# Optimization experiments

Hardware: AMD Instinct MI355X
Metric: run time of the kernel (lower is better)

The kernel has to match this reference:

```python
import jax, jax.numpy as jnp
import numpy as np

N = 50000   # nodes
E = 800000  # edges
D = 128     # input feature dim
HID = 64    # hidden dim
NEG_SLOPE = 0.2


def setup_inputs() -> dict:
    key = jax.random.key(0)
    ks = jax.random.split(key, 12)
    s = 0.1
    x = jax.random.normal(ks[0], (N, D), jnp.float32)
    edge_index = jax.random.randint(ks[1], (2, E), 0, N, dtype=jnp.int64)
    # layer 1: GATConv(128 -> 64, heads=2, concat=False)
    W1 = jax.random.normal(ks[2], (D, 2 * HID), jnp.float32) * s
    a_src1 = jax.random.normal(ks[3], (2, HID), jnp.float32) * s
    a_dst1 = jax.random.normal(ks[4], (2, HID), jnp.float32) * s
    b1 = jnp.zeros((HID,), jnp.float32)
    # layer 2: GATConv(64 -> 64, heads=1, concat=False)
    W2 = jax.random.normal(ks[5], (HID, HID), jnp.float32) * s
    a_src2 = jax.random.normal(ks[6], (1, HID), jnp.float32) * s
    a_dst2 = jax.random.normal(ks[7], (1, HID), jnp.float32) * s
    b2 = jnp.zeros((HID,), jnp.float32)
    # classifier Linear(64 -> 2)
    Wc = jax.random.normal(ks[8], (HID, 2), jnp.float32) * s
    bc = jnp.zeros((2,), jnp.float32)
    return {"x": x, "edge_index": edge_index, "W1": W1, "a_src1": a_src1,
            "a_dst1": a_dst1, "b1": b1, "W2": W2, "a_src2": a_src2,
            "a_dst2": a_dst2, "b2": b2, "Wc": Wc, "bc": bc}


def _gat_layer(x, src, dst, W, a_s, a_d, b, n):
    """PyG GATConv (concat=False -> mean over heads), eval mode."""
    H, C = a_s.shape
    h = (x @ W).reshape(n, H, C)                      # [N,H,C]
    alpha_s = jnp.sum(h * a_s, axis=-1)               # [N,H]
    alpha_d = jnp.sum(h * a_d, axis=-1)               # [N,H]
    e = jax.nn.leaky_relu(alpha_s[src] + alpha_d[dst], NEG_SLOPE)  # [E,H]
    # segment softmax over incoming edges of each target node
    m = jax.ops.segment_max(e, dst, num_segments=n)   # [N,H]
    e = jnp.exp(e - m[dst])
    denom = jax.ops.segment_sum(e, dst, num_segments=n)
    alpha = e / (denom[dst] + 1e-16)                  # [E,H]
    msg = h[src] * alpha[:, :, None]                  # [E,H,C]
    out = jax.ops.segment_sum(msg, dst, num_segments=n)  # [N,H,C]
    return out.mean(axis=1) + b                       # [N,C]


def reference(x, edge_index, W1, a_src1, a_dst1, b1, W2, a_src2, a_dst2, b2, Wc, bc):
    n = x.shape[0]
    loops = jnp.arange(n, dtype=edge_index.dtype)     # PyG add_self_loops=True
    src = jnp.concatenate([edge_index[0], loops])
    dst = jnp.concatenate([edge_index[1], loops])
    h = jax.nn.elu(_gat_layer(x, src, dst, W1, a_src1, a_dst1, b1, n))
    h = jax.nn.elu(_gat_layer(h, src, dst, W2, a_src2, a_dst2, b2, n))
    logits = h @ Wc + bc
    return jax.nn.log_softmax(logits, axis=1)
```

## Files before the change

kernel.cpp:

```cpp
#include <hip/hip_runtime.h>
#include <math.h>

#define NN 50000
#define NE 800000
#define NT (NE + NN)
#define NBUCK 196
#define BE 4096
#define NBLK_B ((NT + BE - 1) / BE)
#define CAP 6144
#define NBLK_G ((NN + 63) / 64)

typedef short bf16x8 __attribute__((ext_vector_type(8)));
typedef float f32x4 __attribute__((ext_vector_type(4)));
union U16x8 { uint4 u; bf16x8 s; };

__device__ __forceinline__ unsigned pk_bf16x2(float x, float y) {
  unsigned ux = __float_as_uint(x); ux = ux + 0x7FFFu + ((ux >> 16) & 1u);
  unsigned uy = __float_as_uint(y); uy = uy + 0x7FFFu + ((uy >> 16) & 1u);
  return (ux >> 16) | (uy & 0xFFFF0000u);
}
__device__ __forceinline__ unsigned short bf16_1(float x) {
  unsigned u = __float_as_uint(x); u = u + 0x7FFFu + ((u >> 16) & 1u);
  return (unsigned short)(u >> 16);
}
__device__ __forceinline__ float blo(unsigned v) { return __uint_as_float(v << 16); }
__device__ __forceinline__ float bhi(unsigned v) { return __uint_as_float(v & 0xFFFF0000u); }

__global__ __launch_bounds__(256) void k_prep(const float* __restrict__ W1, const float* __restrict__ W2,
                                              unsigned short* __restrict__ w1f,
                                              unsigned short* __restrict__ w2f,
                                              int* __restrict__ bcur) {
  int i = blockIdx.x * 256 + threadIdx.x;
  if (i < NBUCK) bcur[i] = i * CAP;
  if (i < 128 * 128) {
    int k = i >> 7, col = i & 127;
    int ct = col >> 4, kt = k >> 5, lane = (((k >> 3) & 3) << 4) | (col & 15), j = k & 7;
    w1f[(((ct << 2) | kt) * 64 + lane) * 8 + j] = bf16_1(W1[i]);
  } else if (i < 128 * 128 + 64 * 64) {
    int e = i - 128 * 128;
    int k = e >> 6, col = e & 63;
    int ct = col >> 4, kt = k >> 5, lane = (((k >> 3) & 3) << 4) | (col & 15), j = k & 7;
    w2f[(((ct << 1) | kt) * 64 + lane) * 8 + j] = bf16_1(W2[e]);
  }
}

__global__ __launch_bounds__(256) void k_gb(
    const int* __restrict__ src, const int* __restrict__ dst,
    int* __restrict__ bcur, unsigned* __restrict__ staging,
    const float* __restrict__ x, const unsigned short* __restrict__ w1f,
    const float* __restrict__ asw_g, const float* __restrict__ adw_g,
    unsigned short* __restrict__ h1b, float* __restrict__ as1, float* __restrict__ ad1) {
  __shared__ int hist[NBUCK];
  __shared__ int base[NBUCK];
  if (blockIdx.x < NBLK_B) {
    const int t = threadIdx.x;
    const int e0 = blockIdx.x * BE;
    if (t < NBUCK) hist[t] = 0;
    __syncthreads();
    for (int j = t; j < BE; j += 256) {
      int i = e0 + j;
      if (i >= NT) break;
      int d = (i < NE) ? dst[i] : (i - NE);
      atomicAdd(&hist[d >> 8], 1);
    }
    __syncthreads();
    if (t < NBUCK) {
      int c = hist[t];
      base[t] = c ? atomicAdd(&bcur[t], c) : 0;
      hist[t] = 0;
    }
    __syncthreads();
    for (int j = t; j < BE; j += 256) {
      int i = e0 + j;
      if (i >= NT) break;
      int s, d;
      if (i < NE) { s = src[i]; d = dst[i]; } else { s = d = i - NE; }
      int b = d >> 8;
      int off = atomicAdd(&hist[b], 1);
      staging[base[b] + off] = ((unsigned)d << 16) | (unsigned)s;
    }
    return;
  }
  const int bid = blockIdx.x - NBLK_B;
  const int t = threadIdx.x;
  const int wid = t >> 6, l = t & 63;
  const int lr = l & 15, lg = l >> 4;
  const int arow = bid * 64 + wid * 16 + lr;
  const bool aok = arow < NN;

  float asw_t[8], adw_t[8];
#pragma unroll
  for (int ct = 0; ct < 8; ++ct) {
    asw_t[ct] = asw_g[ct * 16 + lr];
    adw_t[ct] = adw_g[ct * 16 + lr];
  }

  f32x4 acc[8];
#pragma unroll
  for (int ct = 0; ct < 8; ++ct) acc[ct] = (f32x4){0.f, 0.f, 0.f, 0.f};

#pragma unroll
  for (int kt = 0; kt < 4; ++kt) {
    U16x8 a;
    if (aok) {
      const float* xp = &x[(long long)arow * 128 + kt * 32 + lg * 8];
      float4 f0 = *(const float4*)xp;
      float4 f1 = *(const float4*)(xp + 4);
      a.u.x = pk_bf16x2(f0.x, f0.y); a.u.y = pk_bf16x2(f0.z, f0.w);
      a.u.z = pk_bf16x2(f1.x, f1.y); a.u.w = pk_bf16x2(f1.z, f1.w);
    } else {
      a.u = make_uint4(0, 0, 0, 0);
    }
#pragma unroll
    for (int ct = 0; ct < 8; ++ct) {
      U16x8 b;
      b.u = *(const uint4*)&w1f[(((ct << 2) | kt) * 64 + l) * 8];
      acc[ct] = __builtin_amdgcn_mfma_f32_16x16x32_bf16(a.s, b.s, acc[ct], 0, 0, 0);
    }
  }

  const int gr0 = bid * 64 + wid * 16 + lg * 4;
#pragma unroll
  for (int reg = 0; reg < 4; ++reg) {
    int grow = gr0 + reg;
    bool ok = grow < NN;
    float s0 = 0.f, s1 = 0.f, d0 = 0.f, d1 = 0.f;
#pragma unroll
    for (int ct = 0; ct < 8; ++ct) {
      float v = acc[ct][reg];
      if (ok) h1b[(long long)grow * 128 + ct * 16 + lr] = bf16_1(v);
      if (ct < 4) { s0 += v * asw_t[ct]; d0 += v * adw_t[ct]; }
      else        { s1 += v * asw_t[ct]; d1 += v * adw_t[ct]; }
    }
#pragma unroll
    for (int off = 1; off < 16; off <<= 1) {
      s0 += __shfl_xor(s0, off); d0 += __shfl_xor(d0, off);
      s1 += __shfl_xor(s1, off); d1 += __shfl_xor(d1, off);
    }
    if (ok && lr == 0) {
      as1[grow * 2] = s0; as1[grow * 2 + 1] = s1;
      ad1[grow * 2] = d0; ad1[grow * 2 + 1] = d1;
    }
  }
}

__global__ __launch_bounds__(256) void k_scatter2(const unsigned* __restrict__ staging,
                                                  const int* __restrict__ bcur,
                                                  int* __restrict__ rowptr,
                                                  unsigned short* __restrict__ csr16) {
  __shared__ int lcnt[256];
  __shared__ int wsum[4];
  __shared__ int sOff, sTot;
  const int b = blockIdx.x;
  const int t = threadIdx.x;
  const int nlo = b << 8;
  const int l = t & 63, w = t >> 6;

  int bc = (t < NBUCK) ? bcur[t] - t * CAP : 0;
  int sc = bc;
#pragma unroll
  for (int off = 1; off < 64; off <<= 1) {
    int u = __shfl_up(sc, off);
    if (l >= off) sc += u;
  }
  if (l == 63) wsum[w] = sc;
  __syncthreads();
  {
    int wo = 0;
    for (int i = 0; i < w; ++i) wo += wsum[i];
    int incl = sc + wo;
    if (t == b) sOff = incl - bc;
    if (t == 255) sTot = incl;
  }
  lcnt[t] = 0;
  __syncthreads();

  const int s0 = b * CAP;
  const int cnt = bcur[b] - s0;
  for (int k = t; k < cnt; k += 256)
    atomicAdd(&lcnt[(int)(staging[s0 + k] >> 16) - nlo], 1);
  __syncthreads();
  int v = lcnt[t];
  int sc2 = v;
#pragma unroll
  for (int off = 1; off < 64; off <<= 1) {
    int u = __shfl_up(sc2, off);
    if (l >= off) sc2 += u;
  }
  __syncthreads();
  if (l == 63) wsum[w] = sc2;
  __syncthreads();
  int wo = 0;
  for (int i = 0; i < w; ++i) wo += wsum[i];
  const int base = sOff + sc2 + wo - v;
  if (nlo + t < NN) rowptr[nlo + t] = base;
  if (b == NBUCK - 1 && t == 0) rowptr[NN] = sTot;
  __syncthreads();
  lcnt[t] = base;
  __syncthreads();
  for (int k = t; k < cnt; k += 256) {
    unsigned e = staging[s0 + k];
    int d = (int)(e >> 16) - nlo;
    int pos = atomicAdd(&lcnt[d], 1);
    csr16[pos] = (unsigned short)(e & 0xFFFFu);
  }
}

__global__ __launch_bounds__(256) void k_gat1(
    const int* __restrict__ rowptr, const unsigned short* __restrict__ csr16,
    const unsigned* __restrict__ h1u, const float2* __restrict__ as1,
    const float2* __restrict__ ad1, const float* __restrict__ b1,
    unsigned* __restrict__ out1b) {
  __shared__ float2 sw[4][2][64];
  const int t = threadIdx.x;
  const int wv = t >> 6;
  const int n = blockIdx.x * 4 + wv;
  if (n >= NN) return;
  const int p = t & 63;
  const int h = p >> 5;
  const int beg = rowptr[n], end = rowptr[n + 1];
  const int deg = end - beg;
  const float2 adn = ad1[n];

  float acc0 = 0.f, acc1 = 0.f;
  float inv;

  if (deg <= 64) {
    int s = 0; float e0 = -1e30f, e1 = -1e30f;
    if (p < deg) {
      s = csr16[beg + p];
      float2 a = as1[s];
      e0 = a.x + adn.x; e0 = fmaxf(e0, 0.2f * e0);
      e1 = a.y + adn.y; e1 = fmaxf(e1, 0.2f * e1);
    }
    float m0 = e0, m1 = e1;
#pragma unroll
    for (int off = 1; off < 64; off <<= 1) {
      m0 = fmaxf(m0, __shfl_xor(m0, off));
      m1 = fmaxf(m1, __shfl_xor(m1, off));
    }
    float w0 = (p < deg) ? __expf(e0 - m0) : 0.f;
    float w1 = (p < deg) ? __expf(e1 - m1) : 0.f;
    float d0 = w0, d1 = w1;
#pragma unroll
    for (int off = 1; off < 64; off <<= 1) {
      d0 += __shfl_xor(d0, off);
      d1 += __shfl_xor(d1, off);
    }
    sw[wv][0][p] = make_float2(__int_as_float(s), w0);
    sw[wv][1][p] = make_float2(__int_as_float(s), w1);
    __builtin_amdgcn_wave_barrier();
    inv = 1.f / ((h ? d1 : d0) + 1e-16f);

    int j = 0;
    for (; j + 8 <= deg; j += 8) {
      float2 a[8]; unsigned v[8];
#pragma unroll
      for (int u = 0; u < 8; ++u) a[u] = sw[wv][h][j + u];
#pragma unroll
      for (int u = 0; u < 8; ++u) v[u] = h1u[(__float_as_int(a[u].x) << 6) + p];
#pragma unroll
      for (int u = 0; u < 8; ++u) {
        acc0 += a[u].y * blo(v[u]);
        acc1 += a[u].y * bhi(v[u]);
      }
    }
    if (j + 4 <= deg) {
      float2 a[4]; unsigned v[4];
#pragma unroll
      for (int u = 0; u < 4; ++u) a[u] = sw[wv][h][j + u];
#pragma unroll
      for (int u = 0; u < 4; ++u) v[u] = h1u[(__float_as_int(a[u].x) << 6) + p];
#pragma unroll
      for (int u = 0; u < 4; ++u) {
        acc0 += a[u].y * blo(v[u]);
        acc1 += a[u].y * bhi(v[u]);
      }
      j += 4;
    }
    for (; j < deg; ++j) {
      float2 a = sw[wv][h][j];
      unsigned v = h1u[(__float_as_int(a.x) << 6) + p];
      acc0 += a.y * blo(v); acc1 += a.y * bhi(v);
    }
  } else {
    float m0 = -1e30f, d0 = 0.f, m1 = -1e30f, d1 = 0.f;
    for (int k = beg + p; k < end; k += 64) {
      float2 a = as1[csr16[k]];
      float e0 = a.x + adn.x; e0 = fmaxf(e0, 0.2f * e0);
      float e1 = a.y + adn.y; e1 = fmaxf(e1, 0.2f * e1);
      if (e0 > m0) { d0 *= __expf(m0 - e0); m0 = e0; }
      d0 += __expf(e0 - m0);
      if (e1 > m1) { d1 *= __expf(m1 - e1); m1 = e1; }
      d1 += __expf(e1 - m1);
    }
#pragma unroll
    for (int off = 1; off < 64; off <<= 1) {
      float mo = __shfl_xor(m0, off), dd = __shfl_xor(d0, off);
      float mn = fmaxf(m0, mo);
      d0 = d0 * __expf(m0 - mn) + dd * __expf(mo - mn);
      m0 = mn;
      mo = __shfl_xor(m1, off); dd = __shfl_xor(d1, off);
      mn = fmaxf(m1, mo);
      d1 = d1 * __expf(m1 - mn) + dd * __expf(mo - mn);
      m1 = mn;
    }
    inv = 1.f / ((h ? d1 : d0) + 1e-16f);
    for (int c0 = beg; c0 < end; c0 += 64) {
      int nc = end - c0; if (nc > 64) nc = 64;
      int s = 0; float w0 = 0.f, w1 = 0.f;
      if (p < nc) {
        s = csr16[c0 + p];
        float2 a = as1[s];
        float e0 = a.x + adn.x; e0 = fmaxf(e0, 0.2f * e0);
        float e1 = a.y + adn.y; e1 = fmaxf(e1, 0.2f * e1);
        w0 = __expf(e0 - m0);
        w1 = __expf(e1 - m1);
      }
      __builtin_amdgcn_wave_barrier();
      sw[wv][0][p] = make_float2(__int_as_float(s), w0);
      sw[wv][1][p] = make_float2(__int_as_float(s), w1);
      __builtin_amdgcn_wave_barrier();
      for (int j = 0; j < nc; ++j) {
        float2 a = sw[wv][h][j];
        unsigned v = h1u[(__float_as_int(a.x) << 6) + p];
        acc0 += a.y * blo(v); acc1 += a.y * bhi(v);
      }
      __builtin_amdgcn_wave_barrier();
    }
  }

  acc0 *= inv; acc1 *= inv;
  acc0 += __shfl_xor(acc0, 32);
  acc1 += __shfl_xor(acc1, 32);
  if (p < 32) {
    float u0 = 0.5f * acc0 + b1[2 * p];
    float u1 = 0.5f * acc1 + b1[2 * p + 1];
    u0 = u0 > 0.f ? u0 : expm1f(u0);
    u1 = u1 > 0.f ? u1 : expm1f(u1);
    out1b[n * 32 + p] = pk_bf16x2(u0, u1);
  }
}

__global__ __launch_bounds__(256) void k_gemm2(
    const unsigned short* __restrict__ in_b, const unsigned short* __restrict__ w2f,
    const float* __restrict__ asw_g, const float* __restrict__ adw_g,
    unsigned short* __restrict__ h2b, float* __restrict__ as2, float* __restrict__ ad2) {
  const int t = threadIdx.x;
  const int wid = t >> 6, l = t & 63;
  const int lr = l & 15, lg = l >> 4;
  const int arow = blockIdx.x * 64 + wid * 16 + lr;
  const bool aok = arow < NN;

  float asw_t[4], adw_t[4];
#pragma unroll
  for (int ct = 0; ct < 4; ++ct) {
    asw_t[ct] = asw_g[ct * 16 + lr];
    adw_t[ct] = adw_g[ct * 16 + lr];
  }

  f32x4 acc[4];
#pragma unroll
  for (int ct = 0; ct < 4; ++ct) acc[ct] = (f32x4){0.f, 0.f, 0.f, 0.f};

#pragma unroll
  for (int kt = 0; kt < 2; ++kt) {
    U16x8 a;
    if (aok) a.u = *(const uint4*)&in_b[(long long)arow * 64 + kt * 32 + lg * 8];
    else a.u = make_uint4(0, 0, 0, 0);
#pragma unroll
    for (int ct = 0; ct < 4; ++ct) {
      U16x8 b;
      b.u = *(const uint4*)&w2f[(((ct << 1) | kt) * 64 + l) * 8];
      acc[ct] = __builtin_amdgcn_mfma_f32_16x16x32_bf16(a.s, b.s, acc[ct], 0, 0, 0);
    }
  }

  const int gr0 = blockIdx.x * 64 + wid * 16 + lg * 4;
#pragma unroll
  for (int reg = 0; reg < 4; ++reg) {
    int grow = gr0 + reg;
    bool ok = grow < NN;
    float s0 = 0.f, d0 = 0.f;
#pragma unroll
    for (int ct = 0; ct < 4; ++ct) {
      float v = acc[ct][reg];
      if (ok) h2b[(long long)grow * 64 + ct * 16 + lr] = bf16_1(v);
      s0 += v * asw_t[ct]; d0 += v * adw_t[ct];
    }
#pragma unroll
    for (int off = 1; off < 16; off <<= 1) {
      s0 += __shfl_xor(s0, off); d0 += __shfl_xor(d0, off);
    }
    if (ok && lr == 0) { as2[grow] = s0; ad2[grow] = d0; }
  }
}

__global__ __launch_bounds__(256) void k_gat2(
    const int* __restrict__ rowptr, const unsigned short* __restrict__ csr16,
    const unsigned* __restrict__ h2u, const float* __restrict__ as2,
    const float* __restrict__ ad2, const float* __restrict__ b2,
    const float* __restrict__ Wc, const float* __restrict__ bc,
    float* __restrict__ out) {
  __shared__ float2 sw[4][64];
  const int t = threadIdx.x;
  const int wv = t >> 6;
  const int n = blockIdx.x * 4 + wv;
  if (n >= NN) return;
  const int p = t & 63;
  const int half = p >> 5;
  const int q = p & 31;
  const int beg = rowptr[n], end = rowptr[n + 1];
  const int deg = end - beg;
  const float adn = ad2[n];

  float acc0 = 0.f, acc1 = 0.f;
  float inv;

  if (deg <= 64) {
    int s = 0; float e = -1e30f;
    if (p < deg) {
      s = csr16[beg + p];
      e = as2[s] + adn;
      e = fmaxf(e, 0.2f * e);
    }
    float m = e;
#pragma unroll
    for (int off = 1; off < 64; off <<= 1) m = fmaxf(m, __shfl_xor(m, off));
    float w = (p < deg) ? __expf(e - m) : 0.f;
    float d = w;
#pragma unroll
    for (int off = 1; off < 64; off <<= 1) d += __shfl_xor(d, off);
    sw[wv][p] = make_float2(__int_as_float(s), w);
    __builtin_amdgcn_wave_barrier();
    inv = 1.f / (d + 1e-16f);

    int niter = (deg + 1) >> 1;
    int i = 0;
    for (; i + 4 <= niter; i += 4) {
      float2 a[4]; unsigned v[4];
#pragma unroll
      for (int u = 0; u < 4; ++u) a[u] = sw[wv][2 * (i + u) + half];
#pragma unroll
      for (int u = 0; u < 4; ++u) v[u] = h2u[(__float_as_int(a[u].x) << 5) + q];
#pragma unroll
      for (int u = 0; u < 4; ++u) {
        acc0 += a[u].y * blo(v[u]);
        acc1 += a[u].y * bhi(v[u]);
      }
    }
    if (i + 2 <= niter) {
      float2 a0 = sw[wv][2 * i + half];
      float2 a1 = sw[wv][2 * (i + 1) + half];
      unsigned v0 = h2u[(__float_as_int(a0.x) << 5) + q];
      unsigned v1 = h2u[(__float_as_int(a1.x) << 5) + q];
      acc0 += a0.y * blo(v0); acc1 += a0.y * bhi(v0);
      acc0 += a1.y * blo(v1); acc1 += a1.y * bhi(v1);
      i += 2;
    }
    if (i < niter) {
      float2 a = sw[wv][2 * i + half];
      unsigned v = h2u[(__float_as_int(a.x) << 5) + q];
      acc0 += a.y * blo(v); acc1 += a.y * bhi(v);
    }
  } else {
    float m = -1e30f, d = 0.f;
    for (int k = beg + p; k < end; k += 64) {
      float e = as2[csr16[k]] + adn;
      e = fmaxf(e, 0.2f * e);
      if (e > m) { d *= __expf(m - e); m = e; }
      d += __expf(e - m);
    }
#pragma unroll
    for (int off = 1; off < 64; off <<= 1) {
      float mo = __shfl_xor(m, off), dd = __shfl_xor(d, off);
      float mn = fmaxf(m, mo);
      d = d * __expf(m - mn) + dd * __expf(mo - mn);
      m = mn;
    }
    inv = 1.f / (d + 1e-16f);
    for (int c0 = beg; c0 < end; c0 += 64) {
      int nc = end - c0; if (nc > 64) nc = 64;
      int s = 0; float w = 0.f;
      if (p < nc) {
        s = csr16[c0 + p];
        float e = as2[s] + adn;
        e = fmaxf(e, 0.2f * e);
        w = __expf(e - m);
      }
      __builtin_amdgcn_wave_barrier();
      sw[wv][p] = make_float2(__int_as_float(s), w);
      __builtin_amdgcn_wave_barrier();
      int niter = (nc + 1) >> 1;
      for (int i = 0; i < niter; ++i) {
        int j = 2 * i + half;
        float2 a = sw[wv][j < nc ? j : 0];
        float wj = (j < nc) ? a.y : 0.f;
        unsigned v = h2u[(__float_as_int(a.x) << 5) + q];
        acc0 += wj * blo(v); acc1 += wj * bhi(v);
      }
      __builtin_amdgcn_wave_barrier();
    }
  }

  acc0 += __shfl_xor(acc0, 32);
  acc1 += __shfl_xor(acc1, 32);
  float v0 = acc0 * inv + b2[2 * q];
  float v1 = acc1 * inv + b2[2 * q + 1];
  v0 = v0 > 0.f ? v0 : expm1f(v0);
  v1 = v1 > 0.f ? v1 : expm1f(v1);
  float l0 = v0 * Wc[4 * q] + v1 * Wc[4 * q + 2];
  float l1 = v0 * Wc[4 * q + 1] + v1 * Wc[4 * q + 3];
#pragma unroll
  for (int off = 1; off < 32; off <<= 1) {
    l0 += __shfl_xor(l0, off);
    l1 += __shfl_xor(l1, off);
  }
  if (p == 0) {
    l0 += bc[0]; l1 += bc[1];
    float mx = fmaxf(l0, l1);
    float lse = mx + logf(expf(l0 - mx) + expf(l1 - mx));
    out[n * 2] = l0 - lse;
    out[n * 2 + 1] = l1 - lse;
  }
}

extern "C" void kernel_launch(void* const* d_in, const int* in_sizes, int n_in,
                              void* d_out, int out_size, void* d_ws, size_t ws_size,
                              hipStream_t stream) {
  const float* x    = (const float*)d_in[0];
  const int*   ei   = (const int*)d_in[1];
  const float* W1   = (const float*)d_in[2];
  const float* as1w = (const float*)d_in[3];
  const float* ad1w = (const float*)d_in[4];
  const float* b1   = (const float*)d_in[5];
  const float* W2   = (const float*)d_in[6];
  const float* as2w = (const float*)d_in[7];
  const float* ad2w = (const float*)d_in[8];
  const float* b2   = (const float*)d_in[9];
  const float* Wc   = (const float*)d_in[10];
  const float* bc   = (const float*)d_in[11];
  float* out = (float*)d_out;

  const int* src = ei;
  const int* dst = ei + NE;

  char* p = (char*)d_ws;
  unsigned short* h1b = (unsigned short*)p; p += sizeof(unsigned short) * (long long)NN * 128;
  unsigned short* out1b = (unsigned short*)p; p += sizeof(unsigned short) * (long long)NN * 64;
  unsigned short* h2b = (unsigned short*)p; p += sizeof(unsigned short) * (long long)NN * 64;
  float* as1  = (float*)p; p += sizeof(float) * NN * 2;
  float* ad1  = (float*)p; p += sizeof(float) * NN * 2;
  float* as2  = (float*)p; p += sizeof(float) * NN;
  float* ad2  = (float*)p; p += sizeof(float) * NN;
  int* rowptr  = (int*)p; p += sizeof(int) * (NN + 64);
  int* bcur    = (int*)p; p += sizeof(int) * ((NBUCK + 63) & ~63);
  unsigned* staging = (unsigned*)p; p += sizeof(unsigned) * (long long)NBUCK * CAP;
  unsigned short* csr16 = (unsigned short*)p; p += sizeof(unsigned short) * (long long)NT;
  unsigned short* w1f = (unsigned short*)p; p += sizeof(unsigned short) * 128 * 128;
  unsigned short* w2f = (unsigned short*)p; p += sizeof(unsigned short) * 64 * 64;

  k_prep<<<(128 * 128 + 64 * 64 + 255) / 256, 256, 0, stream>>>(W1, W2, w1f, w2f, bcur);
  k_gb<<<NBLK_B + NBLK_G, 256, 0, stream>>>(src, dst, bcur, staging,
                                            x, w1f, as1w, ad1w, h1b, as1, ad1);
  k_scatter2<<<NBUCK, 256, 0, stream>>>(staging, bcur, rowptr, csr16);

  k_gat1<<<(NN + 3) / 4, 256, 0, stream>>>(rowptr, csr16, (const unsigned*)h1b,
                                           (const float2*)as1, (const float2*)ad1, b1,
                                           (unsigned*)out1b);

  k_gemm2<<<(NN + 63) / 64, 256, 0, stream>>>(out1b, w2f, as2w, ad2w, h2b, as2, ad2);
  k_gat2<<<(NN + 3) / 4, 256, 0, stream>>>(rowptr, csr16, (const unsigned*)h2b,
                                           as2, ad2, b2, Wc, bc, out);
}
```

Before: 114.8 us.

## Fold layer-2 GEMM into aggregation by reassociating linear transform after message passing

Removes the separate layer-2 GEMM kernel by using linearity: attention logits come from out1 dotted with precomputed W2·a vectors (computed in k_prep and applied in k_gat1), and k_gat2 aggregates layer-1 outputs directly, then multiplies the aggregated row by W2 held in shared memory. This saves a kernel launch and the write and re-read of the h2 intermediate. In exchange, each k_gat2 block loads 16KB of W2 into LDS and does a 64x64 matvec per node. Rounding changes slightly because aggregation now uses bf16 out1 values rather than bf16 h2.

```diff
diff --git a/kernel.cpp b/kernel.cpp
--- a/kernel.cpp
+++ b/kernel.cpp
@@ -27,20 +27,26 @@
 __device__ __forceinline__ float bhi(unsigned v) { return __uint_as_float(v & 0xFFFF0000u); }
 
 __global__ __launch_bounds__(256) void k_prep(const float* __restrict__ W1, const float* __restrict__ W2,
+                                              const float* __restrict__ as2w, const float* __restrict__ ad2w,
                                               unsigned short* __restrict__ w1f,
-                                              unsigned short* __restrict__ w2f,
+                                              float* __restrict__ va, float* __restrict__ vd,
                                               int* __restrict__ bcur) {
   int i = blockIdx.x * 256 + threadIdx.x;
   if (i < NBUCK) bcur[i] = i * CAP;
+  if (i < 64) {
+    float sva = 0.f, svd = 0.f;
+#pragma unroll 8
+    for (int c = 0; c < 64; ++c) {
+      float w = W2[i * 64 + c];
+      sva += w * as2w[c];
+      svd += w * ad2w[c];
+    }
+    va[i] = sva; vd[i] = svd;
+  }
   if (i < 128 * 128) {
     int k = i >> 7, col = i & 127;
     int ct = col >> 4, kt = k >> 5, lane = (((k >> 3) & 3) << 4) | (col & 15), j = k & 7;
     w1f[(((ct << 2) | kt) * 64 + lane) * 8 + j] = bf16_1(W1[i]);
-  } else if (i < 128 * 128 + 64 * 64) {
-    int e = i - 128 * 128;
-    int k = e >> 6, col = e & 63;
-    int ct = col >> 4, kt = k >> 5, lane = (((k >> 3) & 3) << 4) | (col & 15), j = k & 7;
-    w2f[(((ct << 1) | kt) * 64 + lane) * 8 + j] = bf16_1(W2[e]);
   }
 }
 
@@ -210,7 +216,8 @@
     const int* __restrict__ rowptr, const unsigned short* __restrict__ csr16,
     const unsigned* __restrict__ h1u, const float2* __restrict__ as1,
     const float2* __restrict__ ad1, const float* __restrict__ b1,
-    unsigned* __restrict__ out1b) {
+    const float* __restrict__ va, const float* __restrict__ vd,
+    unsigned* __restrict__ out1b, float* __restrict__ as2, float* __restrict__ ad2) {
   __shared__ float2 sw[4][2][64];
   const int t = threadIdx.x;
   const int wv = t >> 6;
@@ -333,80 +340,37 @@
   acc0 *= inv; acc1 *= inv;
   acc0 += __shfl_xor(acc0, 32);
   acc1 += __shfl_xor(acc1, 32);
-  if (p < 32) {
-    float u0 = 0.5f * acc0 + b1[2 * p];
-    float u1 = 0.5f * acc1 + b1[2 * p + 1];
-    u0 = u0 > 0.f ? u0 : expm1f(u0);
-    u1 = u1 > 0.f ? u1 : expm1f(u1);
-    out1b[n * 32 + p] = pk_bf16x2(u0, u1);
-  }
-}
-
-__global__ __launch_bounds__(256) void k_gemm2(
-    const unsigned short* __restrict__ in_b, const unsigned short* __restrict__ w2f,
-    const float* __restrict__ asw_g, const float* __restrict__ adw_g,
-    unsigned short* __restrict__ h2b, float* __restrict__ as2, float* __restrict__ ad2) {
-  const int t = threadIdx.x;
-  const int wid = t >> 6, l = t & 63;
-  const int lr = l & 15, lg = l >> 4;
-  const int arow = blockIdx.x * 64 + wid * 16 + lr;
-  const bool aok = arow < NN;
-
-  float asw_t[4], adw_t[4];
-#pragma unroll
-  for (int ct = 0; ct < 4; ++ct) {
-    asw_t[ct] = asw_g[ct * 16 + lr];
-    adw_t[ct] = adw_g[ct * 16 + lr];
-  }
-
-  f32x4 acc[4];
-#pragma unroll
-  for (int ct = 0; ct < 4; ++ct) acc[ct] = (f32x4){0.f, 0.f, 0.f, 0.f};
-
-#pragma unroll
-  for (int kt = 0; kt < 2; ++kt) {
-    U16x8 a;
-    if (aok) a.u = *(const uint4*)&in_b[(long long)arow * 64 + kt * 32 + lg * 8];
-    else a.u = make_uint4(0, 0, 0, 0);
-#pragma unroll
-    for (int ct = 0; ct < 4; ++ct) {
-      U16x8 b;
-      b.u = *(const uint4*)&w2f[(((ct << 1) | kt) * 64 + l) * 8];
-      acc[ct] = __builtin_amdgcn_mfma_f32_16x16x32_bf16(a.s, b.s, acc[ct], 0, 0, 0);
-    }
-  }
-
-  const int gr0 = blockIdx.x * 64 + wid * 16 + lg * 4;
-#pragma unroll
-  for (int reg = 0; reg < 4; ++reg) {
-    int grow = gr0 + reg;
-    bool ok = grow < NN;
-    float s0 = 0.f, d0 = 0.f;
-#pragma unroll
-    for (int ct = 0; ct < 4; ++ct) {
-      float v = acc[ct][reg];
-      if (ok) h2b[(long long)grow * 64 + ct * 16 + lr] = bf16_1(v);
-      s0 += v * asw_t[ct]; d0 += v * adw_t[ct];
-    }
-#pragma unroll
-    for (int off = 1; off < 16; off <<= 1) {
-      s0 += __shfl_xor(s0, off); d0 += __shfl_xor(d0, off);
-    }
-    if (ok && lr == 0) { as2[grow] = s0; ad2[grow] = d0; }
-  }
+  const int pp = p & 31;
+  float u0 = 0.5f * acc0 + b1[2 * pp];
+  float u1 = 0.5f * acc1 + b1[2 * pp + 1];
+  u0 = u0 > 0.f ? u0 : expm1f(u0);
+  u1 = u1 > 0.f ? u1 : expm1f(u1);
+  if (p < 32) out1b[n * 32 + pp] = pk_bf16x2(u0, u1);
+  float vs = u0 * va[2 * pp] + u1 * va[2 * pp + 1];
+  float vdd = u0 * vd[2 * pp] + u1 * vd[2 * pp + 1];
+#pragma unroll
+  for (int off = 1; off < 32; off <<= 1) {
+    vs += __shfl_xor(vs, off);
+    vdd += __shfl_xor(vdd, off);
+  }
+  if (p == 0) { as2[n] = vs; ad2[n] = vdd; }
 }
 
 __global__ __launch_bounds__(256) void k_gat2(
     const int* __restrict__ rowptr, const unsigned short* __restrict__ csr16,
-    const unsigned* __restrict__ h2u, const float* __restrict__ as2,
+    const unsigned* __restrict__ o1u, const float* __restrict__ as2,
     const float* __restrict__ ad2, const float* __restrict__ b2,
-    const float* __restrict__ Wc, const float* __restrict__ bc,
-    float* __restrict__ out) {
+    const float* __restrict__ W2, const float* __restrict__ Wc,
+    const float* __restrict__ bc, float* __restrict__ out) {
   __shared__ float2 sw[4][64];
+  __shared__ float aggL[4][64];
+  __shared__ float w2s[64][64];
   const int t = threadIdx.x;
+  for (int i = t; i < 64 * 64; i += 256) ((float*)w2s)[i] = W2[i];
+  __syncthreads();
+
   const int wv = t >> 6;
   const int n = blockIdx.x * 4 + wv;
-  if (n >= NN) return;
   const int p = t & 63;
   const int half = p >> 5;
   const int q = p & 31;
@@ -442,7 +406,7 @@
 #pragma unroll
       for (int u = 0; u < 4; ++u) a[u] = sw[wv][2 * (i + u) + half];
 #pragma unroll
-      for (int u = 0; u < 4; ++u) v[u] = h2u[(__float_as_int(a[u].x) << 5) + q];
+      for (int u = 0; u < 4; ++u) v[u] = o1u[(__float_as_int(a[u].x) << 5) + q];
 #pragma unroll
       for (int u = 0; u < 4; ++u) {
         acc0 += a[u].y * blo(v[u]);
@@ -452,15 +416,15 @@
     if (i + 2 <= niter) {
       float2 a0 = sw[wv][2 * i + half];
       float2 a1 = sw[wv][2 * (i + 1) + half];
-      unsigned v0 = h2u[(__float_as_int(a0.x) << 5) + q];
-      unsigned v1 = h2u[(__float_as_int(a1.x) << 5) + q];
+      unsigned v0 = o1u[(__float_as_int(a0.x) << 5) + q];
+      unsigned v1 = o1u[(__float_as_int(a1.x) << 5) + q];
       acc0 += a0.y * blo(v0); acc1 += a0.y * bhi(v0);
       acc0 += a1.y * blo(v1); acc1 += a1.y * bhi(v1);
       i += 2;
     }
     if (i < niter) {
       float2 a = sw[wv][2 * i + half];
-      unsigned v = h2u[(__float_as_int(a.x) << 5) + q];
+      unsigned v = o1u[(__float_as_int(a.x) << 5) + q];
       acc0 += a.y * blo(v); acc1 += a.y * bhi(v);
     }
   } else {
@@ -496,7 +460,7 @@
         int j = 2 * i + half;
         float2 a = sw[wv][j < nc ? j : 0];
         float wj = (j < nc) ? a.y : 0.f;
-        unsigned v = h2u[(__float_as_int(a.x) << 5) + q];
+        unsigned v = o1u[(__float_as_int(a.x) << 5) + q];
         acc0 += wj * blo(v); acc1 += wj * bhi(v);
       }
       __builtin_amdgcn_wave_barrier();
@@ -505,14 +469,20 @@
 
   acc0 += __shfl_xor(acc0, 32);
   acc1 += __shfl_xor(acc1, 32);
-  float v0 = acc0 * inv + b2[2 * q];
-  float v1 = acc1 * inv + b2[2 * q + 1];
-  v0 = v0 > 0.f ? v0 : expm1f(v0);
-  v1 = v1 > 0.f ? v1 : expm1f(v1);
-  float l0 = v0 * Wc[4 * q] + v1 * Wc[4 * q + 2];
-  float l1 = v0 * Wc[4 * q + 1] + v1 * Wc[4 * q + 3];
-#pragma unroll
-  for (int off = 1; off < 32; off <<= 1) {
+  if (p < 32) {
+    aggL[wv][2 * q] = acc0 * inv;
+    aggL[wv][2 * q + 1] = acc1 * inv;
+  }
+  __builtin_amdgcn_wave_barrier();
+
+  float hsum = 0.f;
+#pragma unroll 8
+  for (int c = 0; c < 64; ++c) hsum += aggL[wv][c] * w2s[c][p];
+  float v = hsum + b2[p];
+  v = v > 0.f ? v : expm1f(v);
+  float l0 = v * Wc[2 * p], l1 = v * Wc[2 * p + 1];
+#pragma unroll
+  for (int off = 1; off < 64; off <<= 1) {
     l0 += __shfl_xor(l0, off);
     l1 += __shfl_xor(l1, off);
   }
@@ -548,28 +518,27 @@
   char* p = (char*)d_ws;
   unsigned short* h1b = (unsigned short*)p; p += sizeof(unsigned short) * (long long)NN * 128;
   unsigned short* out1b = (unsigned short*)p; p += sizeof(unsigned short) * (long long)NN * 64;
-  unsigned short* h2b = (unsigned short*)p; p += sizeof(unsigned short) * (long long)NN * 64;
   float* as1  = (float*)p; p += sizeof(float) * NN * 2;
   float* ad1  = (float*)p; p += sizeof(float) * NN * 2;
   float* as2  = (float*)p; p += sizeof(float) * NN;
   float* ad2  = (float*)p; p += sizeof(float) * NN;
   int* rowptr  = (int*)p; p += sizeof(int) * (NN + 64);
   int* bcur    = (int*)p; p += sizeof(int) * ((NBUCK + 63) & ~63);
+  float* va    = (float*)p; p += sizeof(float) * 64;
+  float* vd    = (float*)p; p += sizeof(float) * 64;
   unsigned* staging = (unsigned*)p; p += sizeof(unsigned) * (long long)NBUCK * CAP;
   unsigned short* csr16 = (unsigned short*)p; p += sizeof(unsigned short) * (long long)NT;
   unsigned short* w1f = (unsigned short*)p; p += sizeof(unsigned short) * 128 * 128;
-  unsigned short* w2f = (unsigned short*)p; p += sizeof(unsigned short) * 64 * 64;
-
-  k_prep<<<(128 * 128 + 64 * 64 + 255) / 256, 256, 0, stream>>>(W1, W2, w1f, w2f, bcur);
+
+  k_prep<<<(128 * 128 + 255) / 256, 256, 0, stream>>>(W1, W2, as2w, ad2w, w1f, va, vd, bcur);
   k_gb<<<NBLK_B + NBLK_G, 256, 0, stream>>>(src, dst, bcur, staging,
                                             x, w1f, as1w, ad1w, h1b, as1, ad1);
   k_scatter2<<<NBUCK, 256, 0, stream>>>(staging, bcur, rowptr, csr16);
 
   k_gat1<<<(NN + 3) / 4, 256, 0, stream>>>(rowptr, csr16, (const unsigned*)h1b,
                                            (const float2*)as1, (const float2*)ad1, b1,
-                                           (unsigned*)out1b);
-
-  k_gemm2<<<(NN + 63) / 64, 256, 0, stream>>>(out1b, w2f, as2w, ad2w, h2b, as2, ad2);
-  k_gat2<<<(NN + 3) / 4, 256, 0, stream>>>(rowptr, csr16, (const unsigned*)h2b,
-                                           as2, ad2, b2, Wc, bc, out);
-}
+                                           va, vd, (unsigned*)out1b, as2, ad2);
+
+  k_gat2<<<NN / 4, 256, 0, stream>>>(rowptr, csr16, (const unsigned*)out1b,
+                                     as2, ad2, b2, W2, Wc, bc, out);
+}
```

Result: slower. 132.2 us (+15.1%).
